# Kernel optimization log

Measured on AMD Instinct MI355X. Metric: run time of the kernel, lower is better.

Reference implementation:

```python
import jax, jax.numpy as jnp
import numpy as np

N_NODES = 30000
N_EDGES = 480000
IN_CH = 64
CHANNELS = [64, 64, 64]
N_HEADS = 4
BN_EPS = 1e-5


def setup_inputs() -> dict:
    key = jax.random.key(0)
    ks = jax.random.split(key, 32)
    x = jax.random.normal(ks[0], (N_NODES, IN_CH), dtype=jnp.float32)
    # edges with no self loops (module removes then re-adds self loops)
    src = jax.random.randint(ks[1], (N_EDGES,), 0, N_NODES)
    off = jax.random.randint(ks[2], (N_EDGES,), 1, N_NODES)
    dst = (src + off) % N_NODES
    edge_index = jnp.stack([src, dst]).astype(jnp.int64)

    inp = {"x": x, "edge_index": edge_index}
    in_ch = IN_CH
    ki = 3
    for li, out_ch in enumerate(CHANNELS):
        # torch init: uniform_ for linear/u weights, N(0, 0.1) for c and bias
        inp[f"W{li}"] = jax.random.uniform(ks[ki], (out_ch * N_HEADS, in_ch), dtype=jnp.float32)
        inp[f"U{li}"] = jax.random.uniform(ks[ki + 1], (N_HEADS, in_ch), dtype=jnp.float32)
        inp[f"c{li}"] = 0.1 * jax.random.normal(ks[ki + 2], (N_HEADS,), dtype=jnp.float32)
        inp[f"b{li}"] = 0.1 * jax.random.normal(ks[ki + 3], (out_ch,), dtype=jnp.float32)
        if li < len(CHANNELS) - 1:  # BN only between layers
            inp[f"g{li}"] = jnp.ones((out_ch,), dtype=jnp.float32)
            inp[f"bt{li}"] = jnp.zeros((out_ch,), dtype=jnp.float32)
        ki += 4
        in_ch = out_ch
    return inp


def _feast_conv(x, src, dst, W, U, c, b, n_nodes):
    """FeatureSteeredConvolution with mean aggregation (trans-invariant attention)."""
    xi = x[dst]  # central nodes  [E, in]
    xj = x[src]  # neighbors      [E, in]
    logits = (xi - xj) @ U.T + c            # [E, M]
    attn = jax.nn.softmax(logits, axis=1)   # [E, M]
    e = src.shape[0]
    out_ch = W.shape[0] // N_HEADS
    xjw = (xj @ W.T).reshape(e, N_HEADS, out_ch)       # [E, M, out]
    msg = jnp.einsum('em,emo->eo', attn, xjw)           # [E, out]
    agg = jax.ops.segment_sum(msg, dst, num_segments=n_nodes)
    cnt = jax.ops.segment_sum(jnp.ones((e,), msg.dtype), dst, num_segments=n_nodes)
    return agg / cnt[:, None] + b  # self loops guarantee cnt >= 1


def _batch_norm(x, gamma, beta):
    # BatchNorm1d, training mode: biased batch statistics
    mu = x.mean(axis=0)
    var = x.var(axis=0)
    return (x - mu) * jax.lax.rsqrt(var + BN_EPS) * gamma + beta


def reference(x, edge_index, W0, U0, c0, b0, g0, bt0, W1, U1, c1, b1, g1, bt1, W2, U2, c2, b2):
    n = x.shape[0]
    loops = jnp.arange(n, dtype=edge_index.dtype)
    src = jnp.concatenate([edge_index[0], loops])
    dst = jnp.concatenate([edge_index[1], loops])
    h = _feast_conv(x, src, dst, W0, U0, c0, b0, n)
    h = _batch_norm(jax.nn.relu(h), g0, bt0)
    h = _feast_conv(h, src, dst, W1, U1, c1, b1, n)
    h = _batch_norm(jax.nn.relu(h), g1, bt1)
    return _feast_conv(h, src, dst, W2, U2, c2, b2, n)
```

## Files before the change

### kernel.cpp

```cpp
#include <hip/hip_runtime.h>

#define NN 30000
#define NE 480000
#define BN_EPS 1e-5f
#define EBLK 1875
#define FBLK 3750
#define PKBLK 469
#define NSHARD 16

typedef __attribute__((ext_vector_type(8))) short bf16x8;
typedef __attribute__((ext_vector_type(4))) float f32x4;

__device__ __forceinline__ unsigned short f2bf(float x) {
    unsigned int u = __float_as_uint(x);
    return (unsigned short)((u + 0x7fffu + ((u >> 16) & 1u)) >> 16);
}
__device__ __forceinline__ float bf2f(unsigned short h) {
    return __uint_as_float(((unsigned int)h) << 16);
}

__device__ __forceinline__ int detect64(const unsigned int* __restrict__ ei) {
    unsigned int v = ei[1] | ei[3] | ei[5] | ei[7] |
                     ei[9] | ei[11] | ei[13] | ei[15];
    return v == 0u;
}
__device__ __forceinline__ int load_idx(const void* ei, int is64, int pos) {
    if (is64) return (int)((const long long*)ei)[pos];
    return ((const int*)ei)[pos];
}

__global__ __launch_bounds__(256) void k_prep(const float* __restrict__ x,
                                              const float* __restrict__ W0,
                                              const float* __restrict__ W1,
                                              const float* __restrict__ W2,
                                              ushort* __restrict__ xbf,
                                              int4* __restrict__ zerobase,
                                              ushort* __restrict__ wb) {
    int t = blockIdx.x * 256 + threadIdx.x;
    if (t < 480000) {
        float4 v = reinterpret_cast<const float4*>(x)[t];
        ushort4 o;
        o.x = f2bf(v.x); o.y = f2bf(v.y); o.z = f2bf(v.z); o.w = f2bf(v.w);
        reinterpret_cast<ushort4*>(xbf)[t] = o;
    } else if (t < 480000 + 16024) {
        zerobase[t - 480000] = make_int4(0, 0, 0, 0);
    } else if (t < 480000 + 16024 + 49152) {
        int t2 = t - (480000 + 16024);
        int layer = t2 >> 14;
        int r = t2 & 16383;
        int ot = r >> 12;
        int kb = (r >> 9) & 7;
        int l = (r >> 3) & 63;
        int e = r & 7;
        int k = kb * 32 + (l >> 4) * 8 + e;
        int o = ot * 16 + (l & 15);
        int m = k >> 6;
        int kk = k & 63;
        const float* W = (layer == 0) ? W0 : (layer == 1) ? W1 : W2;
        wb[t2] = f2bf(W[(m * 64 + o) * 64 + kk]);
    }
}

__global__ __launch_bounds__(256) void k_hist(const void* __restrict__ ei,
                                              int* __restrict__ degi) {
    int e = blockIdx.x * 256 + threadIdx.x;
    int is64 = detect64((const unsigned int*)ei);
    int d = load_idx(ei, is64, NE + e);
    atomicAdd(&degi[d], 1);
}

__global__ __launch_bounds__(1024) void k_scan(const int* __restrict__ degi,
                                               int* __restrict__ rowptr) {
    __shared__ int sm[1024];
    const int PER = 30;
    int t = threadIdx.x;
    int base = t * PER;
    int loc[PER];
    int sum = 0;
#pragma unroll
    for (int i = 0; i < PER; ++i) {
        int idx = base + i;
        int d = (idx < NN) ? degi[idx] : 0;
        loc[i] = sum;
        sum += d;
    }
    sm[t] = sum;
    __syncthreads();
    for (int off = 1; off < 1024; off <<= 1) {
        int add = (t >= off) ? sm[t - off] : 0;
        __syncthreads();
        sm[t] += add;
        __syncthreads();
    }
    int tb = sm[t] - sum;
#pragma unroll
    for (int i = 0; i < PER; ++i) {
        int idx = base + i;
        if (idx < NN) rowptr[idx] = tb + loc[i];
    }
    if (t == 0) rowptr[NN] = NE;
}

__device__ __forceinline__ void dev_pk0(const float* __restrict__ h,
                                        const float* __restrict__ U,
                                        float* __restrict__ pout, int vb) {
    __shared__ float usc_s[4][64];
    int t = threadIdx.x;
    {
        int m = t >> 6, k = t & 63;
        usc_s[m][k] = U[m * 64 + k];
    }
    __syncthreads();
    int idx = vb * 256 + t;
    if (idx < NN * 4) {
        int n = idx >> 2, m = idx & 3;
        const float4* hn = reinterpret_cast<const float4*>(h) + (size_t)n * 16;
        const float* um = usc_s[m];
        float a = 0.0f;
#pragma unroll
        for (int j = 0; j < 16; ++j) {
            float4 hv = hn[j];
            a += hv.x * um[4 * j + 0] + hv.y * um[4 * j + 1] +
                 hv.z * um[4 * j + 2] + hv.w * um[4 * j + 3];
        }
        pout[idx] = a;
    }
}

__global__ __launch_bounds__(256) void k_scatter_pk0(const void* __restrict__ ei,
                                                     const int* __restrict__ rowptr,
                                                     int* __restrict__ cursor,
                                                     int* __restrict__ csr,
                                                     const float* __restrict__ x,
                                                     const float* __restrict__ U0,
                                                     float* __restrict__ p) {
    if (blockIdx.x < EBLK) {
        int is64 = detect64((const unsigned int*)ei);
        int e = blockIdx.x * 256 + threadIdx.x;
        int s = load_idx(ei, is64, e);
        int d = load_idx(ei, is64, NE + e);
        int pos = rowptr[d] + atomicAdd(&cursor[d], 1);
        csr[pos] = s;
    } else {
        dev_pk0(x, U0, p, blockIdx.x - EBLK);
    }
}

__global__ __launch_bounds__(256) void k_pk(const float* __restrict__ h,
                                            const float* __restrict__ U,
                                            const float* __restrict__ statsS,
                                            const float* __restrict__ g,
                                            const float* __restrict__ W,
                                            const float* __restrict__ bt,
                                            float* __restrict__ pout,
                                            float* __restrict__ cstv_out,
                                            float* __restrict__ scv_out) {
    __shared__ float usc_s[4][64];
    __shared__ float sc_l[64];
    __shared__ float sh_l[64];
    int t = threadIdx.x;
    if (t < 64) {
        float s1 = 0.0f, s2 = 0.0f;
#pragma unroll
        for (int sh = 0; sh < NSHARD; ++sh) {
            s1 += statsS[sh * 128 + t];
            s2 += statsS[sh * 128 + 64 + t];
        }
        const float invN = 1.0f / (float)NN;
        float mu = s1 * invN;
        float var = s2 * invN - mu * mu;
        float sc = rsqrtf(var + BN_EPS) * g[t];
        sc_l[t] = sc;
        sh_l[t] = bt[t] - mu * sc;
        if (blockIdx.x == 0) scv_out[t] = sc;
    }
    __syncthreads();
    {
        int m = t >> 6, k = t & 63;
        usc_s[m][k] = U[m * 64 + k] * sc_l[k];
    }
    __syncthreads();
    int idx = blockIdx.x * 256 + t;
    if (idx < NN * 4) {
        int n = idx >> 2, m = idx & 3;
        const float4* hn = reinterpret_cast<const float4*>(h) + (size_t)n * 16;
        const float* um = usc_s[m];
        float a = 0.0f;
#pragma unroll
        for (int j = 0; j < 16; ++j) {
            float4 hv = hn[j];
            a += hv.x * um[4 * j + 0] + hv.y * um[4 * j + 1] +
                 hv.z * um[4 * j + 2] + hv.w * um[4 * j + 3];
        }
        pout[idx] = a;
    }
    if (blockIdx.x == 0) {
        float s = 0.0f;
        const float* wr = W + (size_t)t * 64;
#pragma unroll 8
        for (int k = 0; k < 64; ++k) s += sh_l[k] * wr[k];
        cstv_out[t] = s;
    }
}

template <int FOLD, int STATS>
__global__ __launch_bounds__(512, 4) void k_fused(const int* __restrict__ rowptr,
                                                  const int* __restrict__ csr,
                                                  const float* __restrict__ p,
                                                  const ushort* __restrict__ hbf_in,
                                                  const float* __restrict__ cvec,
                                                  const float* __restrict__ scv,
                                                  const float* __restrict__ cstvg,
                                                  const ushort* __restrict__ wb,
                                                  const float* __restrict__ bvec,
                                                  float* __restrict__ hout,
                                                  ushort* __restrict__ hbfout,
                                                  float* __restrict__ stats_out) {
    __shared__ float4 attn_s[8][64];
    __shared__ int src_s[8][64];
    __shared__ ushort zrow[8][272];
    __shared__ float4 zs_s[8];
    __shared__ float cstv_s[256];

    int t = threadIdx.x;
    int wid = t >> 6;
    int lane = t & 63;
    int n = blockIdx.x * 8 + wid;
    const float4* p4 = reinterpret_cast<const float4*>(p);

    if (FOLD && t < 256) cstv_s[t] = cstvg[t];

    float scl = FOLD ? scv[lane] : 1.0f;

    float4 cv = make_float4(cvec[0], cvec[1], cvec[2], cvec[3]);
    float smx = fmaxf(fmaxf(cv.x, cv.y), fmaxf(cv.z, cv.w));
    float se0 = __expf(cv.x - smx), se1 = __expf(cv.y - smx);
    float se2 = __expf(cv.z - smx), se3 = __expf(cv.w - smx);
    float sinv = 1.0f / (se0 + se1 + se2 + se3);
    float sl0 = se0 * sinv, sl1 = se1 * sinv, sl2 = se2 * sinv, sl3 = se3 * sinv;

    float4 pd = p4[n];
    float4 pdc = make_float4(pd.x + cv.x, pd.y + cv.y, pd.z + cv.z, pd.w + cv.w);
    float hs = bf2f(hbf_in[(unsigned)(n * 64 + lane)]);
    float acc0 = sl0 * hs, acc1 = sl1 * hs, acc2 = sl2 * hs, acc3 = sl3 * hs;
    float zt0 = sl0, zt1 = sl1, zt2 = sl2, zt3 = sl3;

    int start = rowptr[n];
    int end = rowptr[n + 1];
    for (int j = start; j < end; j += 64) {
        int chunk = end - j;
        if (chunk > 64) chunk = 64;
        if (lane < chunk) {
            int s = csr[j + lane];
            float4 q = p4[(unsigned)s];
            float l0 = pdc.x - q.x;
            float l1 = pdc.y - q.y;
            float l2 = pdc.z - q.z;
            float l3 = pdc.w - q.w;
            float mx = fmaxf(fmaxf(l0, l1), fmaxf(l2, l3));
            float e0 = __expf(l0 - mx);
            float e1 = __expf(l1 - mx);
            float e2 = __expf(l2 - mx);
            float e3 = __expf(l3 - mx);
            float inv = 1.0f / (e0 + e1 + e2 + e3);
            attn_s[wid][lane] = make_float4(e0 * inv, e1 * inv, e2 * inv, e3 * inv);
            src_s[wid][lane] = s;
        }
        int k = 0;
        for (; k + 4 <= chunk; k += 4) {
            float4 a0 = attn_s[wid][k];
            int s0 = src_s[wid][k];
            float4 a1 = attn_s[wid][k + 1];
            int s1 = src_s[wid][k + 1];
            float4 a2 = attn_s[wid][k + 2];
            int s2 = src_s[wid][k + 2];
            float4 a3 = attn_s[wid][k + 3];
            int s3 = src_s[wid][k + 3];
            float h0 = bf2f(hbf_in[(unsigned)(s0 * 64 + lane)]);
            float h1 = bf2f(hbf_in[(unsigned)(s1 * 64 + lane)]);
            float h2 = bf2f(hbf_in[(unsigned)(s2 * 64 + lane)]);
            float h3 = bf2f(hbf_in[(unsigned)(s3 * 64 + lane)]);
            acc0 += a0.x * h0 + a1.x * h1 + a2.x * h2 + a3.x * h3;
            acc1 += a0.y * h0 + a1.y * h1 + a2.y * h2 + a3.y * h3;
            acc2 += a0.z * h0 + a1.z * h1 + a2.z * h2 + a3.z * h3;
            acc3 += a0.w * h0 + a1.w * h1 + a2.w * h2 + a3.w * h3;
            zt0 += a0.x + a1.x + a2.x + a3.x;
            zt1 += a0.y + a1.y + a2.y + a3.y;
            zt2 += a0.z + a1.z + a2.z + a3.z;
            zt3 += a0.w + a1.w + a2.w + a3.w;
        }
        for (; k < chunk; ++k) {
            float4 a0 = attn_s[wid][k];
            int s0 = src_s[wid][k];
            float h0 = bf2f(hbf_in[(unsigned)(s0 * 64 + lane)]);
            acc0 += a0.x * h0;
            acc1 += a0.y * h0;
            acc2 += a0.z * h0;
            acc3 += a0.w * h0;
            zt0 += a0.x; zt1 += a0.y; zt2 += a0.z; zt3 += a0.w;
        }
    }

    float invD = 1.0f / (float)(end - start + 1);
    float s = invD * scl;
    {
        ushort* zr = &zrow[wid][0];
        zr[lane]       = f2bf(acc0 * s);
        zr[64 + lane]  = f2bf(acc1 * s);
        zr[128 + lane] = f2bf(acc2 * s);
        zr[192 + lane] = f2bf(acc3 * s);
        if (lane == 0)
            zs_s[wid] = make_float4(zt0 * invD, zt1 * invD, zt2 * invD, zt3 * invD);
    }
    __syncthreads();

    if (wid >= 4) return;

    int col = lane & 15;
    int grp = lane >> 4;
    int r = (col < 8) ? col : 7;
    const ushort* zr = &zrow[r][0];
    const ushort* wbp = wb + ((size_t)(wid * 8) * 64 + lane) * 8;
    f32x4 acc = {0.0f, 0.0f, 0.0f, 0.0f};
#pragma unroll
    for (int kb = 0; kb < 8; ++kb) {
        bf16x8 a = *reinterpret_cast<const bf16x8*>(zr + kb * 32 + grp * 8);
        bf16x8 b = *reinterpret_cast<const bf16x8*>(wbp + (size_t)kb * 512);
        acc = __builtin_amdgcn_mfma_f32_16x16x32_bf16(a, b, acc, 0, 0, 0);
    }

    float ls = 0.0f, lq = 0.0f;
    if (grp < 2) {
        int n0 = blockIdx.x * 8;
        int o = wid * 16 + col;
        float bval = bvec[o];
#pragma unroll
        for (int i = 0; i < 4; ++i) {
            int nn = n0 + grp * 4 + i;
            float v = acc[i] + bval;
            if (FOLD) {
                float4 zv = zs_s[grp * 4 + i];
                v += zv.x * cstv_s[o] + zv.y * cstv_s[64 + o] +
                     zv.z * cstv_s[128 + o] + zv.w * cstv_s[192 + o];
            }
            if (STATS) {
                v = fmaxf(v, 0.0f);
                hout[(size_t)nn * 64 + o] = v;
                hbfout[(size_t)nn * 64 + o] = f2bf(v);
                ls += v;
                lq += v * v;
            } else {
                hout[(size_t)nn * 64 + o] = v;
            }
        }
        if (STATS) {
            ls += __shfl_xor(ls, 16, 64);
            lq += __shfl_xor(lq, 16, 64);
            if (lane < 16) {
                float* so = stats_out + (blockIdx.x & (NSHARD - 1)) * 128;
                atomicAdd(&so[o], ls);
                atomicAdd(&so[64 + o], lq);
            }
        }
    }
}

extern "C" void kernel_launch(void* const* d_in, const int* in_sizes, int n_in,
                              void* d_out, int out_size, void* d_ws, size_t ws_size,
                              hipStream_t stream) {
    const float* x = (const float*)d_in[0];
    const void* ei = d_in[1];
    const float* W0 = (const float*)d_in[2];
    const float* U0 = (const float*)d_in[3];
    const float* c0 = (const float*)d_in[4];
    const float* b0 = (const float*)d_in[5];
    const float* g0 = (const float*)d_in[6];
    const float* bt0 = (const float*)d_in[7];
    const float* W1 = (const float*)d_in[8];
    const float* U1 = (const float*)d_in[9];
    const float* c1 = (const float*)d_in[10];
    const float* b1 = (const float*)d_in[11];
    const float* g1 = (const float*)d_in[12];
    const float* bt1 = (const float*)d_in[13];
    const float* W2 = (const float*)d_in[14];
    const float* U2 = (const float*)d_in[15];
    const float* c2 = (const float*)d_in[16];
    const float* b2 = (const float*)d_in[17];

    ushort* xbf = (ushort*)d_ws;
    ushort* hbfA = xbf + (size_t)NN * 64;
    ushort* hbfB = hbfA + (size_t)NN * 64;
    float* h = (float*)(hbfB + (size_t)NN * 64);
    float* p = h + (size_t)NN * 64;
    float* cstv = p + (size_t)NN * 4;
    float* scv = cstv + 256;
    int* degi = (int*)(scv + 64);
    int* cursor = degi + NN;
    float* statsA = (float*)(cursor + NN);
    int* rowptr = (int*)(statsA + 4096);
    int* csr = rowptr + NN + 4;
    ushort* wb = (ushort*)(csr + NE);
    float* stats0 = statsA;
    float* stats1 = statsA + 2048;

    const int prepBlocks = (480000 + 16024 + 49152 + 255) / 256;

    k_prep<<<prepBlocks, 256, 0, stream>>>(x, W0, W1, W2, xbf, (int4*)degi, wb);
    k_hist<<<EBLK, 256, 0, stream>>>(ei, degi);
    k_scan<<<1, 1024, 0, stream>>>(degi, rowptr);
    k_scatter_pk0<<<EBLK + PKBLK, 256, 0, stream>>>(ei, rowptr, cursor, csr,
                                                    x, U0, p);

    k_fused<0, 1><<<FBLK, 512, 0, stream>>>(rowptr, csr, p, xbf, c0,
                                            nullptr, nullptr, wb, b0,
                                            h, hbfA, stats0);
    k_pk<<<PKBLK, 256, 0, stream>>>(h, U1, stats0, g0, W1, bt0, p, cstv, scv);
    k_fused<1, 1><<<FBLK, 512, 0, stream>>>(rowptr, csr, p, hbfA, c1,
                                            scv, cstv, wb + 16384, b1,
                                            h, hbfB, stats1);
    k_pk<<<PKBLK, 256, 0, stream>>>(h, U2, stats1, g1, W2, bt1, p, cstv, scv);
    k_fused<1, 0><<<FBLK, 512, 0, stream>>>(rowptr, csr, p, hbfB, c2,
                                            scv, cstv, wb + 32768, b2,
                                            (float*)d_out, nullptr, nullptr);
}
```

Measured before the change: 260.9 us.

## Fuse prep with histogram, reuse degree counter as cursor, drop fp32 hidden writes

Result: no change. 259.2 us (median of 2 runs) (-0.6%).

```diff
diff --git a/kernel.cpp b/kernel.cpp
--- a/kernel.cpp
+++ b/kernel.cpp
@@ -29,23 +29,25 @@
     return ((const int*)ei)[pos];
 }
 
-__global__ __launch_bounds__(256) void k_prep(const float* __restrict__ x,
-                                              const float* __restrict__ W0,
-                                              const float* __restrict__ W1,
-                                              const float* __restrict__ W2,
-                                              ushort* __restrict__ xbf,
-                                              int4* __restrict__ zerobase,
-                                              ushort* __restrict__ wb) {
-    int t = blockIdx.x * 256 + threadIdx.x;
-    if (t < 480000) {
+__global__ __launch_bounds__(256) void k_prep_hist(const float* __restrict__ x,
+                                                   const float* __restrict__ W0,
+                                                   const float* __restrict__ W1,
+                                                   const float* __restrict__ W2,
+                                                   const void* __restrict__ ei,
+                                                   ushort* __restrict__ xbf,
+                                                   ushort* __restrict__ wb,
+                                                   int4* __restrict__ statz,
+                                                   int* __restrict__ degi) {
+    int b = blockIdx.x;
+    int tid = threadIdx.x;
+    if (b < 1875) {
+        int t = b * 256 + tid;
         float4 v = reinterpret_cast<const float4*>(x)[t];
         ushort4 o;
         o.x = f2bf(v.x); o.y = f2bf(v.y); o.z = f2bf(v.z); o.w = f2bf(v.w);
         reinterpret_cast<ushort4*>(xbf)[t] = o;
-    } else if (t < 480000 + 16024) {
-        zerobase[t - 480000] = make_int4(0, 0, 0, 0);
-    } else if (t < 480000 + 16024 + 49152) {
-        int t2 = t - (480000 + 16024);
+    } else if (b < 2067) {
+        int t2 = (b - 1875) * 256 + tid;
         int layer = t2 >> 14;
         int r = t2 & 16383;
         int ot = r >> 12;
@@ -58,31 +60,32 @@
         int kk = k & 63;
         const float* W = (layer == 0) ? W0 : (layer == 1) ? W1 : W2;
         wb[t2] = f2bf(W[(m * 64 + o) * 64 + kk]);
-    }
-}
-
-__global__ __launch_bounds__(256) void k_hist(const void* __restrict__ ei,
-                                              int* __restrict__ degi) {
-    int e = blockIdx.x * 256 + threadIdx.x;
-    int is64 = detect64((const unsigned int*)ei);
-    int d = load_idx(ei, is64, NE + e);
-    atomicAdd(&degi[d], 1);
+    } else if (b < 2071) {
+        statz[(b - 2067) * 256 + tid] = make_int4(0, 0, 0, 0);
+    } else {
+        int e = (b - 2071) * 256 + tid;
+        int is64 = detect64((const unsigned int*)ei);
+        int d = load_idx(ei, is64, NE + e);
+        atomicAdd(&degi[d], 1);
+    }
 }
 
 __global__ __launch_bounds__(1024) void k_scan(const int* __restrict__ degi,
                                                int* __restrict__ rowptr) {
+    __shared__ int buf[30720];
     __shared__ int sm[1024];
+    int t = threadIdx.x;
+    for (int i = t; i < 30720; i += 1024)
+        buf[i] = (i < NN) ? degi[i] : 0;
+    __syncthreads();
     const int PER = 30;
-    int t = threadIdx.x;
     int base = t * PER;
     int loc[PER];
     int sum = 0;
 #pragma unroll
     for (int i = 0; i < PER; ++i) {
-        int idx = base + i;
-        int d = (idx < NN) ? degi[idx] : 0;
         loc[i] = sum;
-        sum += d;
+        sum += buf[base + i];
     }
     sm[t] = sum;
     __syncthreads();
@@ -129,7 +132,7 @@
 
 __global__ __launch_bounds__(256) void k_scatter_pk0(const void* __restrict__ ei,
                                                      const int* __restrict__ rowptr,
-                                                     int* __restrict__ cursor,
+                                                     int* __restrict__ degi,
                                                      int* __restrict__ csr,
                                                      const float* __restrict__ x,
                                                      const float* __restrict__ U0,
@@ -139,14 +142,14 @@
         int e = blockIdx.x * 256 + threadIdx.x;
         int s = load_idx(ei, is64, e);
         int d = load_idx(ei, is64, NE + e);
-        int pos = rowptr[d] + atomicAdd(&cursor[d], 1);
-        csr[pos] = s;
+        int old = atomicSub(&degi[d], 1);
+        csr[rowptr[d] + old - 1] = s;
     } else {
         dev_pk0(x, U0, p, blockIdx.x - EBLK);
     }
 }
 
-__global__ __launch_bounds__(256) void k_pk(const float* __restrict__ h,
+__global__ __launch_bounds__(256) void k_pk(const ushort* __restrict__ hbf,
                                             const float* __restrict__ U,
                                             const float* __restrict__ statsS,
                                             const float* __restrict__ g,
@@ -183,14 +186,20 @@
     int idx = blockIdx.x * 256 + t;
     if (idx < NN * 4) {
         int n = idx >> 2, m = idx & 3;
-        const float4* hn = reinterpret_cast<const float4*>(h) + (size_t)n * 16;
+        const uint4* hn = reinterpret_cast<const uint4*>(hbf + (size_t)n * 64);
         const float* um = usc_s[m];
         float a = 0.0f;
 #pragma unroll
-        for (int j = 0; j < 16; ++j) {
-            float4 hv = hn[j];
-            a += hv.x * um[4 * j + 0] + hv.y * um[4 * j + 1] +
-                 hv.z * um[4 * j + 2] + hv.w * um[4 * j + 3];
+        for (int j = 0; j < 8; ++j) {
+            uint4 v = hn[j];
+            a += bf2f((unsigned short)v.x) * um[8 * j + 0] +
+                 bf2f((unsigned short)(v.x >> 16)) * um[8 * j + 1] +
+                 bf2f((unsigned short)v.y) * um[8 * j + 2] +
+                 bf2f((unsigned short)(v.y >> 16)) * um[8 * j + 3] +
+                 bf2f((unsigned short)v.z) * um[8 * j + 4] +
+                 bf2f((unsigned short)(v.z >> 16)) * um[8 * j + 5] +
+                 bf2f((unsigned short)v.w) * um[8 * j + 6] +
+                 bf2f((unsigned short)(v.w >> 16)) * um[8 * j + 7];
         }
         pout[idx] = a;
     }
@@ -345,7 +354,6 @@
             }
             if (STATS) {
                 v = fmaxf(v, 0.0f);
-                hout[(size_t)nn * 64 + o] = v;
                 hbfout[(size_t)nn * 64 + o] = f2bf(v);
                 ls += v;
                 lq += v * v;
@@ -390,35 +398,32 @@
     ushort* xbf = (ushort*)d_ws;
     ushort* hbfA = xbf + (size_t)NN * 64;
     ushort* hbfB = hbfA + (size_t)NN * 64;
-    float* h = (float*)(hbfB + (size_t)NN * 64);
-    float* p = h + (size_t)NN * 64;
+    float* p = (float*)(hbfB + (size_t)NN * 64);
     float* cstv = p + (size_t)NN * 4;
     float* scv = cstv + 256;
     int* degi = (int*)(scv + 64);
-    int* cursor = degi + NN;
-    float* statsA = (float*)(cursor + NN);
+    float* statsA = (float*)(degi + NN);
     int* rowptr = (int*)(statsA + 4096);
     int* csr = rowptr + NN + 4;
     ushort* wb = (ushort*)(csr + NE);
     float* stats0 = statsA;
     float* stats1 = statsA + 2048;
 
-    const int prepBlocks = (480000 + 16024 + 49152 + 255) / 256;
-
-    k_prep<<<prepBlocks, 256, 0, stream>>>(x, W0, W1, W2, xbf, (int4*)degi, wb);
-    k_hist<<<EBLK, 256, 0, stream>>>(ei, degi);
+    hipMemsetAsync(degi, 0, sizeof(int) * NN, stream);
+    k_prep_hist<<<3946, 256, 0, stream>>>(x, W0, W1, W2, ei, xbf, wb,
+                                          (int4*)statsA, degi);
     k_scan<<<1, 1024, 0, stream>>>(degi, rowptr);
-    k_scatter_pk0<<<EBLK + PKBLK, 256, 0, stream>>>(ei, rowptr, cursor, csr,
+    k_scatter_pk0<<<EBLK + PKBLK, 256, 0, stream>>>(ei, rowptr, degi, csr,
                                                     x, U0, p);
 
     k_fused<0, 1><<<FBLK, 512, 0, stream>>>(rowptr, csr, p, xbf, c0,
                                             nullptr, nullptr, wb, b0,
-                                            h, hbfA, stats0);
-    k_pk<<<PKBLK, 256, 0, stream>>>(h, U1, stats0, g0, W1, bt0, p, cstv, scv);
+                                            nullptr, hbfA, stats0);
+    k_pk<<<PKBLK, 256, 0, stream>>>(hbfA, U1, stats0, g0, W1, bt0, p, cstv, scv);
     k_fused<1, 1><<<FBLK, 512, 0, stream>>>(rowptr, csr, p, hbfA, c1,
                                             scv, cstv, wb + 16384, b1,
-                                            h, hbfB, stats1);
-    k_pk<<<PKBLK, 256, 0, stream>>>(h, U2, stats1, g1, W2, bt1, p, cstv, scv);
+                                            nullptr, hbfB, stats1);
+    k_pk<<<PKBLK, 256, 0, stream>>>(hbfB, U2, stats1, g1, W2, bt1, p, cstv, scv);
     k_fused<1, 0><<<FBLK, 512, 0, stream>>>(rowptr, csr, p, hbfB, c2,
                                             scv, cstv, wb + 32768, b2,
                                             (float*)d_out, nullptr, nullptr);
```
